# Kernel tuning notes

Hardware: AMD Instinct MI355X
Metric: run time of the kernel (lower is better)

## Reference

```python
import jax, jax.numpy as jnp
import numpy as np

B, N, G, K = 4, 2048, 8, 16
C_IN = K * 3 + 3  # in_features_size=0 path: conv1 in = 0 + local_n*3 + 3 = 51
CH = [C_IN, 32, 48, 64, 80, 96]  # feature_size(4i, 4i*3) = 16i for i=2..6
THR = 0.1  # weight_threshold


def setup_inputs() -> dict:
    key = jax.random.key(0)
    ks = jax.random.split(key, 3 + 3 * 5)
    inp = {
        "point_cloud": jax.random.normal(ks[0], (B, N, 3), jnp.float32),
        "normals": jax.random.normal(ks[1], (B, N, 3), jnp.float32),
        "dr_w": jax.random.uniform(ks[2], (B, N, G), jnp.float32),
    }
    for i in range(5):
        cin, cout = CH[i], CH[i + 1]
        k0 = 3 + 3 * i
        inp[f"W{i+1}"] = jax.random.normal(ks[k0], (cin, cout), jnp.float32) * (1.0 / np.sqrt(cin))
        inp[f"b{i+1}"] = jnp.zeros((cout,), jnp.float32)
        inp[f"s{i+1}"] = 1.0 + 0.1 * jax.random.normal(ks[k0 + 1], (cout,), jnp.float32)  # BN (eval) scale
        inp[f"o{i+1}"] = 0.01 * jax.random.normal(ks[k0 + 2], (cout,), jnp.float32)      # BN (eval) shift
    return inp


def _forward(point_cloud, normals, dr_w, params):
    # sign-flip group for full (non rotation-only) 3D frames: 8 ops, flips eigenvector columns
    OPS = jnp.array([[1, 1, 1], [1, 1, -1], [1, -1, 1], [1, -1, -1],
                     [-1, 1, 1], [-1, 1, -1], [-1, -1, 1], [-1, -1, -1]], jnp.float32)
    wn = jnp.swapaxes(dr_w, 1, 2)                                  # [B,G,N]
    wsum = dr_w.sum(1)                                             # [B,G]
    wnorm = dr_w / (dr_w.sum(1, keepdims=True) + 1e-6)             # [B,N,G]
    # --- get_frame (weighted): weighted center + weighted covariance + eigh per group ---
    center = jnp.einsum('bnd,bng->bgd', point_cloud, wnorm)        # [B,G,3]
    pc = point_cloud[:, None, :, :] - center[:, :, None, :]        # [B,G,N,3]
    Rm = jnp.einsum('bgnd,bgn,bgne->bgde', pc, wn, pc)             # [B,G,3,3]
    deg = (wsum > 1.0).astype(Rm.dtype)[..., None, None]           # degenerate-group guard
    noise = jax.random.normal(jax.random.key(42), Rm.shape, Rm.dtype)
    lambdas, V = jnp.linalg.eigh(deg * Rm + (1.0 - deg) * noise)
    frames = jax.lax.stop_gradient(V)                              # is_detach_frame=True
    center = jax.lax.stop_gradient(center)
    F_ops = OPS[None, :, None, None, :] * frames[:, None]          # [B,8,G,3,3]
    # --- soft-weighted kNN over points ---
    ww = jnp.einsum('bng,bmg->bnm', dr_w, dr_w)                    # [B,N,N]
    sq = jnp.sum((point_cloud[:, :, None, :] - point_cloud[:, None, :, :]) ** 2, -1)
    d = ww * sq + (1.0 - ww) * 1000.0
    _, idx = jax.lax.top_k(-d, K)                                  # smallest K -> [B,N,K]
    pnts_n = jax.vmap(lambda p, i: p[i])(point_cloud, idx)         # [B,N,K,3]
    # v1 = (1-w)*center + w*pnts_n - center = w*(pnts_n - center)
    v1 = wn[..., None, None] * (pnts_n[:, None] - center[:, :, None, None, :])  # [B,G,N,K,3]
    # v2: weighted normals blended with per-group weighted mean normal
    nw = normals[:, None, :, :] * wn[..., None]                    # [B,G,N,3]
    nmean = nw.sum(2) / (wsum[..., None] + 1e-6)                   # [B,G,3]
    v2 = nw + (1.0 - wn)[..., None] * nmean[:, :, None, :]         # [B,G,N,3]
    # apply equivariant frames: (F_ops^T @ v^T)^T == v @ F_ops
    f1 = jnp.einsum('bgnkd,bogde->bognke', v1, F_ops)              # [B,8,G,N,K,3]
    f2 = jnp.einsum('bgnd,bogde->bogne', v2, F_ops)                # [B,8,G,N,3]
    x = jnp.concatenate([f1.reshape(B, 8, G, N, K * 3), f2], -1)   # [B,8,G,N,51]
    # MinkowskiLinear + BN(eval affine) + ReLU stack, applied densely then masked
    for (W, b, s, o) in params:
        x = jax.nn.relu((x @ W + b) * s + o)
    mask = (wn >= THR).astype(x.dtype)[:, None, :, :, None]        # weight_threshold filter
    return x * mask                                                # [B,8,G,N,96]


def reference(point_cloud, normals, dr_w,
              W1, b1, s1, o1, W2, b2, s2, o2, W3, b3, s3, o3,
              W4, b4, s4, o4, W5, b5, s5, o5):
    params = [(W1, b1, s1, o1), (W2, b2, s2, o2), (W3, b3, s3, o3),
              (W4, b4, s4, o4), (W5, b5, s5, o5)]
    return _forward(point_cloud, normals, dr_w, params)
```

## Files before the change

### kernel.cpp

```cpp
#include <hip/hip_runtime.h>
#include <math.h>

#define NPTS 2048
#define BATCH 4
#define NG 8
#define KNN_K 16
#define FR_OFF 512
#define IDX_OFF 1024
#define WOFF_F (IDX_OFF + BATCH * NPTS * KNN_K)
#define WOFF_B (WOFF_F + 22016)
#define FLOATMAX 3.402823466e38f

typedef __attribute__((ext_vector_type(8))) short bf16x8;
typedef __attribute__((ext_vector_type(4))) float f32x4;

__device__ inline unsigned short bf16_rne(float x) {
  unsigned u = __float_as_uint(x);
  u += 0x7FFFu + ((u >> 16) & 1u);
  return (unsigned short)(u >> 16);
}
__device__ inline float bf16_f(unsigned short h) {
  return __uint_as_float(((unsigned)h) << 16);
}

__device__ inline unsigned pack_hl(float h) {
  unsigned u = __float_as_uint(h);
  float rem = h - __uint_as_float(u & 0xffff0000u);
  unsigned v = __float_as_uint(rem);
  v += 0x7fffu + ((v >> 16) & 1u);
  return __builtin_amdgcn_perm(u, v, 0x07060302u);
}

__device__ inline void unpack8(const unsigned* __restrict__ p, bf16x8& ah, bf16x8& al) {
  union U { unsigned u[4]; bf16x8 v; };
  uint4 x = *(const uint4*)p;
  uint4 y = *(const uint4*)(p + 4);
  U a, b;
  a.u[0] = __builtin_amdgcn_perm(x.y, x.x, 0x07060302u);
  a.u[1] = __builtin_amdgcn_perm(x.w, x.z, 0x07060302u);
  a.u[2] = __builtin_amdgcn_perm(y.y, y.x, 0x07060302u);
  a.u[3] = __builtin_amdgcn_perm(y.w, y.z, 0x07060302u);
  b.u[0] = __builtin_amdgcn_perm(x.y, x.x, 0x05040100u);
  b.u[1] = __builtin_amdgcn_perm(x.w, x.z, 0x05040100u);
  b.u[2] = __builtin_amdgcn_perm(y.y, y.x, 0x05040100u);
  b.u[3] = __builtin_amdgcn_perm(y.w, y.z, 0x05040100u);
  ah = a.v;
  al = b.v;
}

__device__ inline float slapy2f(float x, float y) {
  float ax = fabsf(x), ay = fabsf(y);
  float w = fmaxf(ax, ay), z = fminf(ax, ay);
  if (z == 0.f) return w;
  float q = z / w;
  return w * sqrtf(1.f + q * q);
}

__device__ inline void slartgf(float f, float g, float& c, float& s, float& r) {
  if (g == 0.f) { c = 1.f; s = 0.f; r = f; }
  else if (f == 0.f) { c = 0.f; s = (g >= 0.f) ? 1.f : -1.f; r = fabsf(g); }
  else {
    float d = sqrtf(f * f + g * g);
    c = fabsf(f) / d;
    r = (f >= 0.f) ? d : -d;
    s = g / r;
  }
}

__device__ void slaev2f(float a, float b, float c, float& rt1, float& rt2, float& cs1, float& sn1) {
  float sm = a + c, df = a - c, adf = fabsf(df), tb = b + b, ab = fabsf(tb);
  float acmx, acmn;
  if (fabsf(a) > fabsf(c)) { acmx = a; acmn = c; } else { acmx = c; acmn = a; }
  float rt;
  if (adf > ab) { float t = ab / adf; rt = adf * sqrtf(1.f + t * t); }
  else if (adf < ab) { float t = adf / ab; rt = ab * sqrtf(1.f + t * t); }
  else rt = ab * sqrtf(2.f);
  int sgn1;
  if (sm < 0.f) { rt1 = 0.5f * (sm - rt); sgn1 = -1; rt2 = (acmx / rt1) * acmn - (b / rt1) * b; }
  else if (sm > 0.f) { rt1 = 0.5f * (sm + rt); sgn1 = 1; rt2 = (acmx / rt1) * acmn - (b / rt1) * b; }
  else { rt1 = 0.5f * rt; rt2 = -0.5f * rt; sgn1 = 1; }
  float cs; int sgn2;
  if (df >= 0.f) { cs = df + rt; sgn2 = 1; } else { cs = df - rt; sgn2 = -1; }
  float acs = fabsf(cs);
  if (acs > ab) {
    float ct = -tb / cs;
    sn1 = 1.f / sqrtf(1.f + ct * ct);
    cs1 = ct * sn1;
  } else {
    if (ab == 0.f) { cs1 = 1.f; sn1 = 0.f; }
    else {
      float tn = -cs / tb;
      cs1 = 1.f / sqrtf(1.f + tn * tn);
      sn1 = tn * cs1;
    }
  }
  if (sgn1 == sgn2) { float tn = cs1; cs1 = -sn1; sn1 = tn; }
}

__device__ void steqr3(float d[3], float e[2], float Z[3][3]) {
  const float eps = 5.9604645e-08f;
  const float eps2 = eps * eps;
  const float safmin = 1.17549435e-38f;
  const int nmaxit = 90;
  const int n = 3;
  int jtot = 0;
  int l1 = 0;
  while (l1 <= n - 1) {
    if (l1 > 0) e[l1 - 1] = 0.f;
    int m;
    for (m = l1; m <= n - 2; m++) {
      float tst = fabsf(e[m]);
      if (tst == 0.f) break;
      if (tst <= (sqrtf(fabsf(d[m])) * sqrtf(fabsf(d[m + 1]))) * eps) { e[m] = 0.f; break; }
    }
    int l = l1, lend = m;
    l1 = m + 1;
    if (lend == l) continue;
    if (fabsf(d[lend]) < fabsf(d[l])) { int tmp = l; l = lend; lend = tmp; }
    if (lend > l) {
      for (;;) {
        int mm = lend;
        if (l != lend) {
          for (mm = l; mm <= lend - 1; mm++) {
            float tst = e[mm] * e[mm];
            if (tst <= eps2 * fabsf(d[mm]) * fabsf(d[mm + 1]) + safmin) break;
          }
        }
        if (mm < lend) e[mm] = 0.f;
        float p = d[l];
        if (mm == l) {
          d[l] = p; l++;
          if (l <= lend) continue; else break;
        }
        if (mm == l + 1) {
          float rt1, rt2, c, s;
          slaev2f(d[l], e[l], d[l + 1], rt1, rt2, c, s);
          #pragma unroll
          for (int i = 0; i < 3; i++) {
            float tp = Z[i][l + 1];
            Z[i][l + 1] = c * tp - s * Z[i][l];
            Z[i][l] = s * tp + c * Z[i][l];
          }
          d[l] = rt1; d[l + 1] = rt2; e[l] = 0.f;
          l += 2;
          if (l <= lend) continue; else break;
        }
        if (jtot == nmaxit) break;
        jtot++;
        float g = (d[l + 1] - p) / (2.f * e[l]);
        float r = slapy2f(g, 1.f);
        g = d[mm] - p + e[l] / (g + copysignf(r, g));
        float s = 1.f, c = 1.f;
        p = 0.f;
        float cs[2], sn[2];
        for (int i = mm - 1; i >= l; i--) {
          float f = s * e[i];
          float bb = c * e[i];
          slartgf(g, f, c, s, r);
          if (i != mm - 1) e[i + 1] = r;
          g = d[i + 1] - p;
          r = (d[i] - g) * s + 2.f * c * bb;
          p = s * r;
          d[i + 1] = g + p;
          g = c * r - bb;
          cs[i] = c; sn[i] = -s;
        }
        for (int jj = mm - l - 1; jj >= 0; jj--) {
          float c_ = cs[l + jj], s_ = sn[l + jj];
          #pragma unroll
          for (int i = 0; i < 3; i++) {
            float tp = Z[i][l + jj + 1];
            Z[i][l + jj + 1] = c_ * tp - s_ * Z[i][l + jj];
            Z[i][l + jj] = s_ * tp + c_ * Z[i][l + jj];
          }
        }
        d[l] -= p;
        e[l] = g;
      }
    } else {
      for (;;) {
        int mm = lend;
        if (l != lend) {
          for (mm = l; mm >= lend + 1; mm--) {
            float tst = e[mm - 1] * e[mm - 1];
            if (tst <= eps2 * fabsf(d[mm]) * fabsf(d[mm - 1]) + safmin) break;
          }
        }
        if (mm > lend) e[mm - 1] = 0.f;
        float p = d[l];
        if (mm == l) {
          d[l] = p; l--;
          if (l >= lend) continue; else break;
        }
        if (mm == l - 1) {
          float rt1, rt2, c, s;
          slaev2f(d[l - 1], e[l - 1], d[l], rt1, rt2, c, s);
          #pragma unroll
          for (int i = 0; i < 3; i++) {
            float tp = Z[i][l];
            Z[i][l] = c * tp - s * Z[i][l - 1];
            Z[i][l - 1] = s * tp + c * Z[i][l - 1];
          }
          d[l - 1] = rt1; d[l] = rt2; e[l - 1] = 0.f;
          l -= 2;
          if (l >= lend) continue; else break;
        }
        if (jtot == nmaxit) break;
        jtot++;
        float g = (d[l - 1] - p) / (2.f * e[l - 1]);
        float r = slapy2f(g, 1.f);
        g = d[mm] - p + e[l - 1] / (g + copysignf(r, g));
        float s = 1.f, c = 1.f;
        p = 0.f;
        float cs[2], sn[2];
        for (int i = mm; i <= l - 1; i++) {
          float f = s * e[i];
          float bb = c * e[i];
          slartgf(g, f, c, s, r);
          if (i != mm) e[i - 1] = r;
          g = d[i] - p;
          r = (d[i + 1] - g) * s + 2.f * c * bb;
          p = s * r;
          d[i] = g + p;
          g = c * r - bb;
          cs[i] = c; sn[i] = s;
        }
        for (int jj = 0; jj <= l - mm - 1; jj++) {
          float c_ = cs[mm + jj], s_ = sn[mm + jj];
          #pragma unroll
          for (int i = 0; i < 3; i++) {
            float tp = Z[i][mm + jj + 1];
            Z[i][mm + jj + 1] = c_ * tp - s_ * Z[i][mm + jj];
            Z[i][mm + jj] = s_ * tp + c_ * Z[i][mm + jj];
          }
        }
        d[l] -= p;
        e[l - 1] = g;
      }
    }
  }
  for (int ii = 1; ii < 3; ii++) {
    int i = ii - 1, k = i;
    float p = d[i];
    for (int j = ii; j < 3; j++) if (d[j] < p) { k = j; p = d[j]; }
    if (k != i) {
      d[k] = d[i]; d[i] = p;
      for (int r2 = 0; r2 < 3; r2++) {
        float tp = Z[r2][i]; Z[r2][i] = Z[r2][k]; Z[r2][k] = tp;
      }
    }
  }
}

__device__ void eigh_compute(float A00, float A10, float A11, float A20, float A21,
                             float A22, float* __restrict__ fr) {
  float d[3], e[2];
  float tau = 0.f, u2 = 0.f;
  d[0] = A00;
  float alpha = A10, x31 = A20;
  if (x31 == 0.f) {
    tau = 0.f; u2 = 0.f;
    d[1] = A11; d[2] = A22; e[0] = alpha; e[1] = A21;
  } else {
    float nrm = slapy2f(alpha, fabsf(x31));
    float beta = (alpha >= 0.f) ? -nrm : nrm;
    tau = (beta - alpha) / beta;
    u2 = (1.f / (alpha - beta)) * x31;
    float x1 = tau * (A11 + A21 * u2);
    float x2 = tau * (A21 + A22 * u2);
    float al = -0.5f * tau * (x1 + x2 * u2);
    x1 = x1 + al;
    x2 = x2 + al * u2;
    d[1] = A11 - 2.f * x1;
    e[1] = A21 - (u2 * x1 + x2);
    d[2] = A22 - 2.f * (u2 * x2);
    e[0] = beta;
  }

  float Z[3][3] = {{1.f, 0.f, 0.f}, {0.f, 1.f, 0.f}, {0.f, 0.f, 1.f}};
  steqr3(d, e, Z);

  if (tau != 0.f) {
    for (int j = 0; j < 3; j++) {
      float w = Z[1][j] + u2 * Z[2][j];
      float tw = tau * w;
      Z[1][j] -= tw;
      Z[2][j] -= tw * u2;
    }
  }
  for (int dd = 0; dd < 3; dd++)
    for (int ee = 0; ee < 3; ee++)
      fr[dd * 3 + ee] = Z[dd][ee];
}

__global__ __launch_bounds__(256, 4) void front_kernel(
    const float* __restrict__ pc, const float* __restrict__ nrm,
    const float* __restrict__ drw,
    const float* __restrict__ W1, const float* __restrict__ W2,
    const float* __restrict__ W3, const float* __restrict__ W4,
    const float* __restrict__ W5,
    const float* __restrict__ B1, const float* __restrict__ S1, const float* __restrict__ O1,
    const float* __restrict__ B2, const float* __restrict__ S2, const float* __restrict__ O2,
    const float* __restrict__ B3, const float* __restrict__ S3, const float* __restrict__ O3,
    const float* __restrict__ B4, const float* __restrict__ S4, const float* __restrict__ O4,
    const float* __restrict__ B5, const float* __restrict__ S5, const float* __restrict__ O5,
    int* __restrict__ idxout, float* __restrict__ ws) {
  __shared__ float red[256];
  int t = threadIdx.x;

  if (blockIdx.x < 32) {
    int bg = blockIdx.x;
    int b = bg >> 3, g = bg & 7;

    float sw = 0.f, sp0 = 0.f, sp1 = 0.f, sp2 = 0.f, sn0 = 0.f, sn1 = 0.f, sn2 = 0.f;
    for (int n = t; n < NPTS; n += 256) {
      float w = drw[((size_t)b * NPTS + n) * NG + g];
      const float* p = pc + ((size_t)b * NPTS + n) * 3;
      const float* nr = nrm + ((size_t)b * NPTS + n) * 3;
      sw += w;
      sp0 += w * p[0]; sp1 += w * p[1]; sp2 += w * p[2];
      sn0 += w * nr[0]; sn1 += w * nr[1]; sn2 += w * nr[2];
    }

    auto blockReduce = [&](float v) -> float {
      red[t] = v; __syncthreads();
      for (int s = 128; s > 0; s >>= 1) {
        if (t < s) red[t] += red[t + s];
        __syncthreads();
      }
      float r = red[0];
      __syncthreads();
      return r;
    };

    float Sw = blockReduce(sw);
    float inv = 1.f / (Sw + 1e-6f);
    float C0 = blockReduce(sp0) * inv;
    float C1 = blockReduce(sp1) * inv;
    float C2 = blockReduce(sp2) * inv;
    float M0 = blockReduce(sn0) * inv;
    float M1 = blockReduce(sn1) * inv;
    float M2 = blockReduce(sn2) * inv;

    float r00 = 0.f, r10 = 0.f, r11 = 0.f, r20 = 0.f, r21 = 0.f, r22 = 0.f;
    for (int n = t; n < NPTS; n += 256) {
      float w = drw[((size_t)b * NPTS + n) * NG + g];
      const float* p = pc + ((size_t)b * NPTS + n) * 3;
      float p0 = p[0] - C0, p1 = p[1] - C1, p2 = p[2] - C2;
      r00 += w * p0 * p0;
      r10 += w * p1 * p0;
      r11 += w * p1 * p1;
      r20 += w * p2 * p0;
      r21 += w * p2 * p1;
      r22 += w * p2 * p2;
    }
    float R00 = blockReduce(r00);
    float R10 = blockReduce(r10);
    float R11 = blockReduce(r11);
    float R20 = blockReduce(r20);
    float R21 = blockReduce(r21);
    float R22 = blockReduce(r22);

    if (t == 0) {
      float* st = ws + bg * 16;
      st[1] = C0; st[2] = C1; st[3] = C2;
      st[4] = M0; st[5] = M1; st[6] = M2;
      eigh_compute(R00, R10, R11, R20, R21, R22, ws + FR_OFF + bg * 9);
    }
    return;
  }

  if (blockIdx.x < 75) {
    if (t >= 64) return;
    const int FBt[5] = {0, 4, 7, 15, 25};
    const int NTs[5] = {2, 3, 4, 5, 6};
    const int CINs[5] = {51, 32, 48, 64, 80};
    const int COUTs[5] = {32, 48, 64, 80, 96};
    const float* Ws[5] = {W1, W2, W3, W4, W5};
    const float* Ss[5] = {S1, S2, S3, S4, S5};

    int fp = blockIdx.x - 32;
    int layer = 0;
    while (layer < 4 && fp >= FBt[layer + 1]) layer++;
    int rel = fp - FBt[layer];
    int kt = rel / NTs[layer], nt = rel % NTs[layer];
    int lane = t;
    int c = nt * 16 + (lane & 15);
    int q = lane >> 4;
    int cin = CINs[layer], cout = COUTs[layer];
    const float* W = Ws[layer];
    float sc = Ss[layer][c];

    unsigned short* wb = (unsigned short*)(ws + WOFF_F);
    unsigned short* dH = wb + fp * 1024 + lane * 8;
    unsigned short* dL = dH + 512;
    for (int i = 0; i < 8; i++) {
      int k = kt * 32 + q * 8 + i;
      float w = (k < cin) ? W[(size_t)k * cout + c] * sc : 0.f;
      unsigned short hb = bf16_rne(w);
      dH[i] = hb;
      dL[i] = bf16_rne(w - bf16_f(hb));
    }

    if (fp == 0) {
      const int CUM[5] = {0, 32, 80, 144, 224};
      const float* Bs[5] = {B1, B2, B3, B4, B5};
      const float* Os[5] = {O1, O2, O3, O4, O5};
      for (int idx = t; idx < 320; idx += 64) {
        int ly = 4;
        while (ly > 0 && idx < CUM[ly]) ly--;
        int cc = idx - CUM[ly];
        ws[WOFF_B + idx] = fmaf(Bs[ly][cc], Ss[ly][cc], Os[ly][cc]);
      }
    }
    return;
  }

  int lane = t & 63;
  int q = (blockIdx.x - 75) * 4 + (t >> 6);
  int b = q >> 11;
  int n = q & (NPTS - 1);

  const float* qp = pc + ((size_t)b * NPTS + n) * 3;
  float q0 = qp[0], q1 = qp[1], q2 = qp[2];
  const float4* qw4 = (const float4*)(drw + ((size_t)b * NPTS + n) * NG);
  float4 qa = qw4[0], qb = qw4[1];

  float d[32];
  #pragma unroll
  for (int j = 0; j < 32; j++) {
    int m = j * 64 + lane;
    const float4* mw4 = (const float4*)(drw + ((size_t)b * NPTS + m) * NG);
    float4 ma = mw4[0], mb = mw4[1];
    float ww = qa.x * ma.x + qa.y * ma.y + qa.z * ma.z + qa.w * ma.w
             + qb.x * mb.x + qb.y * mb.y + qb.z * mb.z + qb.w * mb.w;
    const float* mp = pc + ((size_t)b * NPTS + m) * 3;
    float dx = q0 - mp[0], dy = q1 - mp[1], dz = q2 - mp[2];
    float sq = dx * dx + dy * dy + dz * dz;
    d[j] = ww * sq + (1.f - ww) * 1000.f;
    if ((j & 3) == 3) __builtin_amdgcn_sched_barrier(0);
  }

  int myres = 0;
  #pragma unroll 1
  for (int r = 0; r < KNN_K; r++) {
    float bd = d[0];
    int bj = 0;
    #pragma unroll
    for (int j = 1; j < 32; j++) {
      if (d[j] < bd) { bd = d[j]; bj = j; }
    }
    int gm = bj * 64 + lane;
    #pragma unroll
    for (int s = 1; s < 64; s <<= 1) {
      float od = __shfl_xor(bd, s, 64);
      int om = __shfl_xor(gm, s, 64);
      if (od < bd || (od == bd && om < gm)) { bd = od; gm = om; }
    }
    if (lane == r) myres = gm;
    int ls = gm & 63, js = gm >> 6;
    if (lane == ls) {
      #pragma unroll
      for (int j = 0; j < 32; j++) {
        if (j == js) d[j] = FLOATMAX;
      }
    }
  }
  if (lane < KNN_K) idxout[(size_t)q * KNN_K + lane] = myres;
}

#define PST0 84
#define PST1 68

template <int CIN, int COUT, int FB, int SIN, int SOUT>
__device__ inline void mfma_layerP(const unsigned short* __restrict__ wfr,
                                   const unsigned* inP, unsigned* outP,
                                   const float* __restrict__ bias, int lane, int wv) {
  constexpr int KT = (CIN + 31) / 32;
  constexpr int NT = COUT / 16;
  int r = lane & 15, q = lane >> 4;
  int arow = (wv * 16 + r) * SIN;

  f32x4 acc[NT];
  #pragma unroll
  for (int i = 0; i < NT; i++) acc[i] = (f32x4){0.f, 0.f, 0.f, 0.f};

  #pragma unroll
  for (int kt = 0; kt < KT; kt++) {
    bf16x8 ah, al;
    unpack8(inP + arow + kt * 32 + q * 8, ah, al);
    #pragma unroll
    for (int nt = 0; nt < NT; nt++) {
      int fid = FB + kt * NT + nt;
      bf16x8 bh = *(const bf16x8*)(wfr + fid * 1024 + lane * 8);
      bf16x8 bl = *(const bf16x8*)(wfr + fid * 1024 + 512 + lane * 8);
      acc[nt] = __builtin_amdgcn_mfma_f32_16x16x32_bf16(ah, bh, acc[nt], 0, 0, 0);
      acc[nt] = __builtin_amdgcn_mfma_f32_16x16x32_bf16(ah, bl, acc[nt], 0, 0, 0);
      acc[nt] = __builtin_amdgcn_mfma_f32_16x16x32_bf16(al, bh, acc[nt], 0, 0, 0);
    }
  }

  #pragma unroll
  for (int nt = 0; nt < NT; nt++) {
    int c = nt * 16 + r;
    float bb = bias[c];
    #pragma unroll
    for (int j = 0; j < 4; j++) {
      float h = fmaxf(acc[nt][j] + bb, 0.f);
      outP[(wv * 16 + q * 4 + j) * SOUT + c] = pack_hl(h);
    }
  }
}

__global__ __launch_bounds__(256, 4) void mlp_kernel(
    const float* __restrict__ pc, const float* __restrict__ nrm, const float* __restrict__ drw,
    const int* __restrict__ kidx, const float* __restrict__ ws,
    float* __restrict__ out) {
  __shared__ __align__(16) unsigned smem[9728];
  unsigned* PK0 = smem;
  unsigned* PK1 = smem + 5376;

  int t = threadIdx.x;
  int bi = blockIdx.x;
  int b = bi >> 11;
  int g = (bi >> 8) & 7;
  int n0 = (bi & 255) << 3;
  int bg = b * 8 + g;

  for (int z = t; z < 1088; z += 256) {
    int row = z / 17;
    int cc = z - row * 17;
    int col = (cc < 13) ? (51 + cc) : (67 + cc);
    PK0[row * PST0 + col] = 0u;
  }
  if (t < 12) PK1[t] = 0u;

  if (t < 128) {
    int i = t >> 4, kk = t & 15;
    int n = n0 + i;
    int id = kidx[((size_t)b * NPTS + n) * KNN_K + kk];
    const float* p = pc + ((size_t)b * NPTS + id) * 3;
    const float* fr = ws + FR_OFF + bg * 9;
    const float* ct = ws + bg * 16 + 1;
    float w = drw[((size_t)b * NPTS + n) * NG + g];
    float v0 = w * (p[0] - ct[0]);
    float v1 = w * (p[1] - ct[1]);
    float v2 = w * (p[2] - ct[2]);
    #pragma unroll
    for (int e = 0; e < 3; e++) {
      float gv = v0 * fr[e] + v1 * fr[3 + e] + v2 * fr[6 + e];
      unsigned pk = pack_hl(gv);
      int f = 3 * kk + e;
      #pragma unroll
      for (int op = 0; op < 8; op++) {
        int sb = (e == 0) ? (op >> 2) : (e == 1) ? (op >> 1) : op;
        unsigned pv = (sb & 1) ? (pk ^ 0x80008000u) : pk;
        PK0[(i * 8 + op) * PST0 + f] = pv;
      }
    }
  } else if (t < 136) {
    int i = t - 128;
    int n = n0 + i;
    float w = drw[((size_t)b * NPTS + n) * NG + g];
    const float* nr = nrm + ((size_t)b * NPTS + n) * 3;
    const float* fr = ws + FR_OFF + bg * 9;
    const float* nm = ws + bg * 16 + 4;
    float v0 = nr[0] * w + (1.f - w) * nm[0];
    float v1 = nr[1] * w + (1.f - w) * nm[1];
    float v2 = nr[2] * w + (1.f - w) * nm[2];
    #pragma unroll
    for (int e = 0; e < 3; e++) {
      float gv = v0 * fr[e] + v1 * fr[3 + e] + v2 * fr[6 + e];
      unsigned pk = pack_hl(gv);
      int f = 48 + e;
      #pragma unroll
      for (int op = 0; op < 8; op++) {
        int sb = (e == 0) ? (op >> 2) : (e == 1) ? (op >> 1) : op;
        unsigned pv = (sb & 1) ? (pk ^ 0x80008000u) : pk;
        PK0[(i * 8 + op) * PST0 + f] = pv;
      }
    }
  }
  __syncthreads();

  const unsigned short* wfr = (const unsigned short*)(ws + WOFF_F);
  const float* bias = ws + WOFF_B;
  int lane = t & 63;
  int wv = t >> 6;

  mfma_layerP<51, 32, 0, PST0, PST1>(wfr, PK0, PK1, bias + 0, lane, wv);
  __builtin_amdgcn_s_barrier();
  mfma_layerP<32, 48, 4, PST1, PST0>(wfr, PK1, PK0, bias + 32, lane, wv);
  __builtin_amdgcn_s_barrier();
  mfma_layerP<48, 64, 7, PST0, PST1>(wfr, PK0, PK1, bias + 80, lane, wv);
  __builtin_amdgcn_s_barrier();
  mfma_layerP<64, 80, 15, PST1, PST0>(wfr, PK1, PK0, bias + 144, lane, wv);
  __builtin_amdgcn_s_barrier();

  {
    constexpr int KT = 3, NT = 6, FB = 25;
    int r = lane & 15, q = lane >> 4;
    int arow = (wv * 16 + r) * PST0;
    f32x4 acc[NT];
    #pragma unroll
    for (int i = 0; i < NT; i++) acc[i] = (f32x4){0.f, 0.f, 0.f, 0.f};
    #pragma unroll
    for (int kt = 0; kt < KT; kt++) {
      bf16x8 ah, al;
      unpack8(PK0 + arow + kt * 32 + q * 8, ah, al);
      #pragma unroll
      for (int nt = 0; nt < NT; nt++) {
        int fid = FB + kt * NT + nt;
        bf16x8 bh = *(const bf16x8*)(wfr + fid * 1024 + lane * 8);
        bf16x8 bl = *(const bf16x8*)(wfr + fid * 1024 + 512 + lane * 8);
        acc[nt] = __builtin_amdgcn_mfma_f32_16x16x32_bf16(ah, bh, acc[nt], 0, 0, 0);
        acc[nt] = __builtin_amdgcn_mfma_f32_16x16x32_bf16(ah, bl, acc[nt], 0, 0, 0);
        acc[nt] = __builtin_amdgcn_mfma_f32_16x16x32_bf16(al, bh, acc[nt], 0, 0, 0);
      }
    }
    int i = 2 * wv + (q >> 1);
    int n = n0 + i;
    float wlane = drw[((size_t)b * NPTS + n) * NG + g];
    float maskv = (wlane >= 0.1f) ? 1.f : 0.f;
    int opbase = (q & 1) * 4;
    const float* b5 = ws + WOFF_B + 224;
    #pragma unroll
    for (int nt = 0; nt < NT; nt++) {
      int c = nt * 16 + r;
      float bb = b5[c];
      #pragma unroll
      for (int j = 0; j < 4; j++) {
        int op = opbase + j;
        float h = fmaxf(acc[nt][j] + bb, 0.f);
        out[((((size_t)(b * 8 + op)) * NG + g) * NPTS + n) * 96 + c] = h * maskv;
      }
    }
  }
}

extern "C" void kernel_launch(void* const* d_in, const int* in_sizes, int n_in,
                              void* d_out, int out_size, void* d_ws, size_t ws_size,
                              hipStream_t stream) {
  const float* pc = (const float*)d_in[0];
  const float* nrm = (const float*)d_in[1];
  const float* drw = (const float*)d_in[2];
  const float* W1 = (const float*)d_in[3];
  const float* B1 = (const float*)d_in[4];
  const float* S1 = (const float*)d_in[5];
  const float* O1 = (const float*)d_in[6];
  const float* W2 = (const float*)d_in[7];
  const float* B2 = (const float*)d_in[8];
  const float* S2 = (const float*)d_in[9];
  const float* O2 = (const float*)d_in[10];
  const float* W3 = (const float*)d_in[11];
  const float* B3 = (const float*)d_in[12];
  const float* S3 = (const float*)d_in[13];
  const float* O3 = (const float*)d_in[14];
  const float* W4 = (const float*)d_in[15];
  const float* B4 = (const float*)d_in[16];
  const float* S4 = (const float*)d_in[17];
  const float* O4 = (const float*)d_in[18];
  const float* W5 = (const float*)d_in[19];
  const float* B5 = (const float*)d_in[20];
  const float* S5 = (const float*)d_in[21];
  const float* O5 = (const float*)d_in[22];
  float* out = (float*)d_out;
  float* wsf = (float*)d_ws;
  int* idxw = (int*)(wsf + IDX_OFF);

  front_kernel<<<75 + BATCH * NPTS / 4, 256, 0, stream>>>(
      pc, nrm, drw, W1, W2, W3, W4, W5,
      B1, S1, O1, B2, S2, O2, B3, S3, O3, B4, S4, O4, B5, S5, O5,
      idxw, wsf);
  mlp_kernel<<<BATCH * NG * (NPTS / 8), 256, 0, stream>>>(
      pc, nrm, drw, idxw, wsf, out);
}
```

Baseline: 370.6 us.

## Process 16 points per MLP block with two M-tiles per wave

Doubles the MLP block tile from 8 to 16 points (128 rows), so each wave computes two 16-row MFMA tiles and reuses each loaded weight fragment for both. This halves the grid and the per-row weight fragment loads from the workspace. In exchange it doubles LDS use per block, raises register pressure, and lowers the launch-bounds occupancy hint from 4 to 2.

```diff
diff --git a/kernel.cpp b/kernel.cpp
--- a/kernel.cpp
+++ b/kernel.cpp
@@ -473,30 +473,38 @@
 #define PST1 68
 
 template <int CIN, int COUT, int FB, int SIN, int SOUT>
-__device__ inline void mfma_layerP(const unsigned short* __restrict__ wfr,
-                                   const unsigned* inP, unsigned* outP,
-                                   const float* __restrict__ bias, int lane, int wv) {
+__device__ inline void mfma_layer32(const unsigned short* __restrict__ wfr,
+                                    const unsigned* inP, unsigned* outP,
+                                    const float* __restrict__ bias, int lane, int wv) {
   constexpr int KT = (CIN + 31) / 32;
   constexpr int NT = COUT / 16;
   int r = lane & 15, q = lane >> 4;
-  int arow = (wv * 16 + r) * SIN;
-
-  f32x4 acc[NT];
+  int arow0 = (wv * 32 + r) * SIN;
+  int arow1 = arow0 + 16 * SIN;
+
+  f32x4 acc0[NT], acc1[NT];
   #pragma unroll
-  for (int i = 0; i < NT; i++) acc[i] = (f32x4){0.f, 0.f, 0.f, 0.f};
+  for (int i = 0; i < NT; i++) {
+    acc0[i] = (f32x4){0.f, 0.f, 0.f, 0.f};
+    acc1[i] = (f32x4){0.f, 0.f, 0.f, 0.f};
+  }
 
   #pragma unroll
   for (int kt = 0; kt < KT; kt++) {
-    bf16x8 ah, al;
-    unpack8(inP + arow + kt * 32 + q * 8, ah, al);
+    bf16x8 ah0, al0, ah1, al1;
+    unpack8(inP + arow0 + kt * 32 + q * 8, ah0, al0);
+    unpack8(inP + arow1 + kt * 32 + q * 8, ah1, al1);
     #pragma unroll
     for (int nt = 0; nt < NT; nt++) {
       int fid = FB + kt * NT + nt;
       bf16x8 bh = *(const bf16x8*)(wfr + fid * 1024 + lane * 8);
       bf16x8 bl = *(const bf16x8*)(wfr + fid * 1024 + 512 + lane * 8);
-      acc[nt] = __builtin_amdgcn_mfma_f32_16x16x32_bf16(ah, bh, acc[nt], 0, 0, 0);
-      acc[nt] = __builtin_amdgcn_mfma_f32_16x16x32_bf16(ah, bl, acc[nt], 0, 0, 0);
-      acc[nt] = __builtin_amdgcn_mfma_f32_16x16x32_bf16(al, bh, acc[nt], 0, 0, 0);
+      acc0[nt] = __builtin_amdgcn_mfma_f32_16x16x32_bf16(ah0, bh, acc0[nt], 0, 0, 0);
+      acc0[nt] = __builtin_amdgcn_mfma_f32_16x16x32_bf16(ah0, bl, acc0[nt], 0, 0, 0);
+      acc0[nt] = __builtin_amdgcn_mfma_f32_16x16x32_bf16(al0, bh, acc0[nt], 0, 0, 0);
+      acc1[nt] = __builtin_amdgcn_mfma_f32_16x16x32_bf16(ah1, bh, acc1[nt], 0, 0, 0);
+      acc1[nt] = __builtin_amdgcn_mfma_f32_16x16x32_bf16(ah1, bl, acc1[nt], 0, 0, 0);
+      acc1[nt] = __builtin_amdgcn_mfma_f32_16x16x32_bf16(al1, bh, acc1[nt], 0, 0, 0);
     }
   }
 
@@ -506,28 +514,30 @@
     float bb = bias[c];
     #pragma unroll
     for (int j = 0; j < 4; j++) {
-      float h = fmaxf(acc[nt][j] + bb, 0.f);
-      outP[(wv * 16 + q * 4 + j) * SOUT + c] = pack_hl(h);
-    }
-  }
-}
-
-__global__ __launch_bounds__(256, 4) void mlp_kernel(
+      float h0 = fmaxf(acc0[nt][j] + bb, 0.f);
+      outP[(wv * 32 + q * 4 + j) * SOUT + c] = pack_hl(h0);
+      float h1 = fmaxf(acc1[nt][j] + bb, 0.f);
+      outP[(wv * 32 + 16 + q * 4 + j) * SOUT + c] = pack_hl(h1);
+    }
+  }
+}
+
+__global__ __launch_bounds__(256, 2) void mlp_kernel(
     const float* __restrict__ pc, const float* __restrict__ nrm, const float* __restrict__ drw,
     const int* __restrict__ kidx, const float* __restrict__ ws,
     float* __restrict__ out) {
-  __shared__ __align__(16) unsigned smem[9728];
+  __shared__ __align__(16) unsigned smem[19456];
   unsigned* PK0 = smem;
-  unsigned* PK1 = smem + 5376;
+  unsigned* PK1 = smem + 10752;
 
   int t = threadIdx.x;
   int bi = blockIdx.x;
-  int b = bi >> 11;
-  int g = (bi >> 8) & 7;
-  int n0 = (bi & 255) << 3;
+  int b = bi >> 10;
+  int g = (bi >> 7) & 7;
+  int n0 = (bi & 127) << 4;
   int bg = b * 8 + g;
 
-  for (int z = t; z < 1088; z += 256) {
+  for (int z = t; z < 2176; z += 256) {
     int row = z / 17;
     int cc = z - row * 17;
     int col = (cc < 13) ? (51 + cc) : (67 + cc);
@@ -535,7 +545,7 @@
   }
   if (t < 12) PK1[t] = 0u;
 
-  if (t < 128) {
+  {
     int i = t >> 4, kk = t & 15;
     int n = n0 + i;
     int id = kidx[((size_t)b * NPTS + n) * KNN_K + kk];
@@ -558,8 +568,9 @@
         PK0[(i * 8 + op) * PST0 + f] = pv;
       }
     }
-  } else if (t < 136) {
-    int i = t - 128;
+  }
+  if (t < 16) {
+    int i = t;
     int n = n0 + i;
     float w = drw[((size_t)b * NPTS + n) * NG + g];
     const float* nr = nrm + ((size_t)b * NPTS + n) * 3;
@@ -588,40 +599,51 @@
   int lane = t & 63;
   int wv = t >> 6;
 
-  mfma_layerP<51, 32, 0, PST0, PST1>(wfr, PK0, PK1, bias + 0, lane, wv);
+  mfma_layer32<51, 32, 0, PST0, PST1>(wfr, PK0, PK1, bias + 0, lane, wv);
   __builtin_amdgcn_s_barrier();
-  mfma_layerP<32, 48, 4, PST1, PST0>(wfr, PK1, PK0, bias + 32, lane, wv);
+  mfma_layer32<32, 48, 4, PST1, PST0>(wfr, PK1, PK0, bias + 32, lane, wv);
   __builtin_amdgcn_s_barrier();
-  mfma_layerP<48, 64, 7, PST0, PST1>(wfr, PK0, PK1, bias + 80, lane, wv);
+  mfma_layer32<48, 64, 7, PST0, PST1>(wfr, PK0, PK1, bias + 80, lane, wv);
   __builtin_amdgcn_s_barrier();
-  mfma_layerP<64, 80, 15, PST1, PST0>(wfr, PK1, PK0, bias + 144, lane, wv);
+  mfma_layer32<64, 80, 15, PST1, PST0>(wfr, PK1, PK0, bias + 144, lane, wv);
   __builtin_amdgcn_s_barrier();
 
   {
     constexpr int KT = 3, NT = 6, FB = 25;
     int r = lane & 15, q = lane >> 4;
-    int arow = (wv * 16 + r) * PST0;
-    f32x4 acc[NT];
-    #pragma unroll
-    for (int i = 0; i < NT; i++) acc[i] = (f32x4){0.f, 0.f, 0.f, 0.f};
+    int arow0 = (wv * 32 + r) * PST0;
+    int arow1 = arow0 + 16 * PST0;
+    f32x4 acc0[NT], acc1[NT];
+    #pragma unroll
+    for (int i = 0; i < NT; i++) {
+      acc0[i] = (f32x4){0.f, 0.f, 0.f, 0.f};
+      acc1[i] = (f32x4){0.f, 0.f, 0.f, 0.f};
+    }
     #pragma unroll
     for (int kt = 0; kt < KT; kt++) {
-      bf16x8 ah, al;
-      unpack8(PK0 + arow + kt * 32 + q * 8, ah, al);
+      bf16x8 ah0, al0, ah1, al1;
+      unpack8(PK0 + arow0 + kt * 32 + q * 8, ah0, al0);
+      unpack8(PK0 + arow1 + kt * 32 + q * 8, ah1, al1);
       #pragma unroll
       for (int nt = 0; nt < NT; nt++) {
         int fid = FB + kt * NT + nt;
         bf16x8 bh = *(const bf16x8*)(wfr + fid * 1024 + lane * 8);
         bf16x8 bl = *(const bf16x8*)(wfr + fid * 1024 + 512 + lane * 8);
-        acc[nt] = __builtin_amdgcn_mfma_f32_16x16x32_bf16(ah, bh, acc[nt], 0, 0, 0);
-        acc[nt] = __builtin_amdgcn_mfma_f32_16x16x32_bf16(ah, bl, acc[nt], 0, 0, 0);
-        acc[nt] = __builtin_amdgcn_mfma_f32_16x16x32_bf16(al, bh, acc[nt], 0, 0, 0);
-      }
-    }
-    int i = 2 * wv + (q >> 1);
-    int n = n0 + i;
-    float wlane = drw[((size_t)b * NPTS + n) * NG + g];
-    float maskv = (wlane >= 0.1f) ? 1.f : 0.f;
+        acc0[nt] = __builtin_amdgcn_mfma_f32_16x16x32_bf16(ah0, bh, acc0[nt], 0, 0, 0);
+        acc0[nt] = __builtin_amdgcn_mfma_f32_16x16x32_bf16(ah0, bl, acc0[nt], 0, 0, 0);
+        acc0[nt] = __builtin_amdgcn_mfma_f32_16x16x32_bf16(al0, bh, acc0[nt], 0, 0, 0);
+        acc1[nt] = __builtin_amdgcn_mfma_f32_16x16x32_bf16(ah1, bh, acc1[nt], 0, 0, 0);
+        acc1[nt] = __builtin_amdgcn_mfma_f32_16x16x32_bf16(ah1, bl, acc1[nt], 0, 0, 0);
+        acc1[nt] = __builtin_amdgcn_mfma_f32_16x16x32_bf16(al1, bh, acc1[nt], 0, 0, 0);
+      }
+    }
+    int i0 = wv * 4 + (q >> 1);
+    int i1 = i0 + 2;
+    int nA = n0 + i0, nB = n0 + i1;
+    float w0 = drw[((size_t)b * NPTS + nA) * NG + g];
+    float w1 = drw[((size_t)b * NPTS + nB) * NG + g];
+    float mask0 = (w0 >= 0.1f) ? 1.f : 0.f;
+    float mask1 = (w1 >= 0.1f) ? 1.f : 0.f;
     int opbase = (q & 1) * 4;
     const float* b5 = ws + WOFF_B + 224;
     #pragma unroll
@@ -631,8 +653,10 @@
       #pragma unroll
       for (int j = 0; j < 4; j++) {
         int op = opbase + j;
-        float h = fmaxf(acc[nt][j] + bb, 0.f);
-        out[((((size_t)(b * 8 + op)) * NG + g) * NPTS + n) * 96 + c] = h * maskv;
+        float h0 = fmaxf(acc0[nt][j] + bb, 0.f);
+        out[((((size_t)(b * 8 + op)) * NG + g) * NPTS + nA) * 96 + c] = h0 * mask0;
+        float h1 = fmaxf(acc1[nt][j] + bb, 0.f);
+        out[((((size_t)(b * 8 + op)) * NG + g) * NPTS + nB) * 96 + c] = h1 * mask1;
       }
     }
   }
@@ -672,6 +696,6 @@
       pc, nrm, drw, W1, W2, W3, W4, W5,
       B1, S1, O1, B2, S2, O2, B3, S3, O3, B4, S4, O4, B5, S5, O5,
       idxw, wsf);
-  mlp_kernel<<<BATCH * NG * (NPTS / 8), 256, 0, stream>>>(
+  mlp_kernel<<<BATCH * NG * (NPTS / 16), 256, 0, stream>>>(
       pc, nrm, drw, idxw, wsf, out);
 }
```

After: 379.2 us. +2.3%, slower.
